# Kernel optimization log

Hardware: AMD Instinct MI355X
Metric: run time of the kernel (lower is better)

The kernel has to match this reference:

```python
import jax, jax.numpy as jnp
import numpy as np

D_MODEL, D_INNER, D_STATE, D_CONV, DT_RANK = 1024, 2048, 16, 4, 64
BATCH, SEQLEN = 4, 2048


def setup_inputs() -> dict:
    key = jax.random.key(0)
    ks = jax.random.split(key, 10)
    def n(k, shape, scale=1.0):
        return (jax.random.normal(k, shape, dtype=jnp.float32) * scale)
    # A_log = log of positive values in (0, d_state] like the torch init
    A_log = jnp.log(jax.random.uniform(ks[7], (D_INNER, D_STATE), dtype=jnp.float32, minval=0.5, maxval=float(D_STATE)))
    return {
        "hidden_states": n(ks[0], (BATCH, SEQLEN, D_MODEL)),
        "in_proj_w": n(ks[1], (2 * D_INNER, D_MODEL), D_MODEL ** -0.5),
        "conv_w": n(ks[2], (D_INNER, D_CONV), D_CONV ** -0.5),
        "conv_b": n(ks[3], (D_INNER,), 0.1),
        "x_proj_w": n(ks[4], (DT_RANK + 2 * D_STATE, D_INNER), D_INNER ** -0.5),
        "dt_proj_w": n(ks[5], (D_INNER, DT_RANK), DT_RANK ** -0.5),
        "dt_proj_b": n(ks[6], (D_INNER,), 0.5),
        "A_log": A_log,
        "D": jnp.ones((D_INNER,), dtype=jnp.float32),
        "out_proj_w": n(ks[8], (D_MODEL, D_INNER), D_INNER ** -0.5),
    }


def _silu(x):
    return x * jax.nn.sigmoid(x)


def _mamba_forward(hidden_states, in_proj_w, conv_w, conv_b, x_proj_w,
                   dt_proj_w, dt_proj_b, A_log, D, out_proj_w):
    B, L, _ = hidden_states.shape
    d_inner, d_conv = conv_w.shape
    d_state = A_log.shape[1]
    dt_rank = dt_proj_w.shape[1]

    # in_proj (no bias): (b, l, 2*d_inner)
    xz = jnp.einsum('bld,ed->ble', hidden_states, in_proj_w)
    x, z = xz[..., :d_inner], xz[..., d_inner:]

    # causal depthwise conv1d (padding = d_conv-1, truncated to L) + SiLU
    x_pad = jnp.pad(x, ((0, 0), (d_conv - 1, 0), (0, 0)))  # (b, L+d_conv-1, d)
    x_conv = sum(x_pad[:, w:w + L, :] * conv_w[:, w] for w in range(d_conv)) + conv_b
    x_conv = _silu(x_conv)  # (b, l, d_inner)

    # x_proj -> dt, B, C
    x_dbl = jnp.einsum('bld,ed->ble', x_conv, x_proj_w)  # (b, l, dt_rank+2*d_state)
    dt_in = x_dbl[..., :dt_rank]
    Bv = x_dbl[..., dt_rank:dt_rank + d_state]  # (b, l, n)
    Cv = x_dbl[..., dt_rank + d_state:]         # (b, l, n)

    delta = jax.nn.softplus(jnp.einsum('blr,dr->bld', dt_in, dt_proj_w) + dt_proj_b)
    A = -jnp.exp(A_log)  # (d, n), entries negative

    # selective scan over time: state h is (b, d, n)
    def step(h, inp):
        d_t, B_t, C_t, u_t = inp  # (b,d), (b,n), (b,n), (b,d)
        dA = jnp.exp(d_t[:, :, None] * A)                          # (b, d, n)
        h = h * dA + (d_t * u_t)[:, :, None] * B_t[:, None, :]     # (b, d, n)
        y = jnp.einsum('bdn,bn->bd', h, C_t)                       # (b, d)
        return h, y

    h0 = jnp.zeros((B, d_inner, d_state), dtype=hidden_states.dtype)
    xs = (jnp.swapaxes(delta, 0, 1), jnp.swapaxes(Bv, 0, 1),
          jnp.swapaxes(Cv, 0, 1), jnp.swapaxes(x_conv, 0, 1))
    _, ys = jax.lax.scan(step, h0, xs)  # (l, b, d)
    y = jnp.swapaxes(ys, 0, 1) + x_conv * D  # skip term D * u
    y = y * _silu(z)                           # gating

    # out_proj (no bias)
    return jnp.einsum('bld,md->blm', y, out_proj_w)


def reference(hidden_states, in_proj_w, conv_w, conv_b, x_proj_w,
              dt_proj_w, dt_proj_b, A_log, D, out_proj_w):
    return _mamba_forward(hidden_states, in_proj_w, conv_w, conv_b, x_proj_w,
                          dt_proj_w, dt_proj_b, A_log, D, out_proj_w)
```

## Files before the change

### kernel.cpp

```cpp
#include <hip/hip_runtime.h>
#include <hip/hip_bf16.h>

constexpr int BATCH = 4, SEQLEN = 2048, DM = 1024, DI = 2048, DS = 16, DC = 4, DTR = 64;
constexpr int M = BATCH * SEQLEN;
constexpr int NXZ = 2 * DI;
constexpr int NXDBL = DTR + 2 * DS;
constexpr int CL = 64;
constexpr int NCH = SEQLEN / CL;
constexpr size_t CS = (size_t)BATCH * DI * DS;
constexpr float L2E = 1.44269504088896f;

typedef __attribute__((ext_vector_type(8))) short short8;
typedef __attribute__((ext_vector_type(4))) float f32x4;

__device__ __forceinline__ float fexp2(float x) { return __builtin_amdgcn_exp2f(x); }
__device__ __forceinline__ float frcp(float x) { return __builtin_amdgcn_rcpf(x); }
__device__ __forceinline__ float fsig(float z) {
  return frcp(1.f + fexp2(-L2E * z));
}
__device__ __forceinline__ float softplus_fast(float x) {
  return (x > 20.f) ? x
                    : 0.693147180559945f * __builtin_amdgcn_logf(1.f + fexp2(x * L2E));
}

__device__ __forceinline__ void load_lds16(const void* g, void* l) {
  __builtin_amdgcn_global_load_lds(
      (const __attribute__((address_space(1))) unsigned int*)g,
      (__attribute__((address_space(3))) unsigned int*)l, 16, 0, 0);
}

__device__ __forceinline__ void vwaitn(int n) {
  switch (n) {
    case 0: asm volatile("s_waitcnt vmcnt(0)" ::: "memory"); break;
    case 2: asm volatile("s_waitcnt vmcnt(2)" ::: "memory"); break;
    case 6: asm volatile("s_waitcnt vmcnt(6)" ::: "memory"); break;
    default: asm volatile("s_waitcnt vmcnt(8)" ::: "memory"); break;
  }
}

__global__ __launch_bounds__(256) void k_cvt(const float* __restrict__ s,
                                             __hip_bfloat16* __restrict__ d, int n) {
  int i = (blockIdx.x * 256 + threadIdx.x) * 4;
  if (i + 3 < n) {
    float4 v = *reinterpret_cast<const float4*>(s + i);
    d[i + 0] = __float2bfloat16(v.x);
    d[i + 1] = __float2bfloat16(v.y);
    d[i + 2] = __float2bfloat16(v.z);
    d[i + 3] = __float2bfloat16(v.w);
  }
}

__global__ __launch_bounds__(256) void k_cvt4(const float* __restrict__ p0, int n0, __hip_bfloat16* __restrict__ q0,
                                              const float* __restrict__ p1, int n1, __hip_bfloat16* __restrict__ q1,
                                              const float* __restrict__ p2, int n2, __hip_bfloat16* __restrict__ q2,
                                              const float* __restrict__ p3, int n3, __hip_bfloat16* __restrict__ q3) {
  int i = (blockIdx.x * 256 + threadIdx.x) * 4;
  const float* s;
  __hip_bfloat16* d;
  if (i < n0) { s = p0; d = q0; }
  else if ((i -= n0) < n1) { s = p1; d = q1; }
  else if ((i -= n1) < n2) { s = p2; d = q2; }
  else if ((i -= n2) < n3) { s = p3; d = q3; }
  else return;
  float4 v = *reinterpret_cast<const float4*>(s + i);
  d[i + 0] = __float2bfloat16(v.x);
  d[i + 1] = __float2bfloat16(v.y);
  d[i + 2] = __float2bfloat16(v.z);
  d[i + 3] = __float2bfloat16(v.w);
}

__global__ __launch_bounds__(256) void k_prepA(const float* __restrict__ alog,
                                               float* __restrict__ an, int n) {
  int i = blockIdx.x * 256 + threadIdx.x;
  if (i < n) an[i] = -__expf(alog[i]) * L2E;
}

__global__ __launch_bounds__(256) void k_prepCW(const float* __restrict__ cw,
                                                float* __restrict__ cwt) {
  int i = blockIdx.x * 256 + threadIdx.x;
  if (i < DI * DC) {
    int d = i >> 2, w = i & 3;
    cwt[w * DI + d] = cw[i];
  }
}

template <int OUTMODE>
__global__ __launch_bounds__(512, 2) void k_gemm8b(const __hip_bfloat16* __restrict__ A, int lda,
                                                   const __hip_bfloat16* __restrict__ Bm, int ldb,
                                                   void* __restrict__ Cp, int ldc, int K) {
  constexpr int BK = 64;
  constexpr int SS = 24576;
  const int tid = threadIdx.x;
  const int wid = tid >> 6, l = tid & 63;
  const int wr = wid >> 2, wc = wid & 3;

  const int gx = gridDim.x;
  int nlin = blockIdx.y * gx + blockIdx.x;
  {
    const int nwg = gx * gridDim.y;
    nlin = (nlin & 7) * (nwg >> 3) + (nlin >> 3);
  }
  const int bm0 = (nlin / gx) * 256, bn0 = (nlin % gx) * 128;
  const int NT = K / BK;

  __shared__ short LDS[3 * SS];

  const int gc8 = (l & 7) ^ ((l >> 3) & 7);
  const __hip_bfloat16* Abase = A + (size_t)(bm0 + wid * 8 + (l >> 3)) * lda + gc8 * 8;
  const __hip_bfloat16* Bbase = Bm + (size_t)(bn0 + wid * 8 + (l >> 3)) * ldb + gc8 * 8;
  const int wslot = wid * 512;

  const int c8k0 = ((l >> 4) ^ (l & 7)) * 8;
  const int c8k1 = ((4 + (l >> 4)) ^ (l & 7)) * 8;
  const int aoff0 = wr * 8192 + (l & 15) * 64;
  const int boff0 = 16384 + (wc * 32 + (l & 15)) * 64;

  f32x4 acc[8][2] = {};
  short8 a[4][2], b[2][2];

  auto stageA = [&](int slot, int kt) {
#pragma unroll
    for (int g = 0; g < 4; g++)
      load_lds16(Abase + (size_t)(g * 64) * lda + kt * BK,
                 &LDS[slot * SS + g * 4096 + wslot]);
  };
  auto stageB = [&](int slot, int kt) {
#pragma unroll
    for (int g = 0; g < 2; g++)
      load_lds16(Bbase + (size_t)(g * 64) * ldb + kt * BK,
                 &LDS[slot * SS + 16384 + g * 4096 + wslot]);
  };

  stageA(0, 0); stageB(0, 0);
  stageA(1, 1); stageB(1, 1);

  for (int t = 0; t < NT; t++) {
    const int slot = t % 3;
    const int sbase = slot * SS;
    const int s2 = (t + 2) % 3;
    const bool pf2 = (t + 2 < NT);
    vwaitn((t + 1 < NT) ? 6 : 0);
    __builtin_amdgcn_s_barrier();
    const int adb = sbase + aoff0;
    const int bdb = sbase + boff0;
#pragma unroll
    for (int i = 0; i < 4; i++) {
      a[i][0] = *reinterpret_cast<const short8*>(&LDS[adb + i * 1024 + c8k0]);
      a[i][1] = *reinterpret_cast<const short8*>(&LDS[adb + i * 1024 + c8k1]);
    }
#pragma unroll
    for (int j = 0; j < 2; j++) {
      b[j][0] = *reinterpret_cast<const short8*>(&LDS[bdb + j * 1024 + c8k0]);
      b[j][1] = *reinterpret_cast<const short8*>(&LDS[bdb + j * 1024 + c8k1]);
    }
    if (pf2) stageA(s2, t + 2);
    __builtin_amdgcn_sched_barrier(0);
    __builtin_amdgcn_s_setprio(1);
#pragma unroll
    for (int i = 0; i < 4; i++)
#pragma unroll
      for (int j = 0; j < 2; j++)
#pragma unroll
        for (int ks = 0; ks < 2; ks++)
          acc[i][j] = __builtin_amdgcn_mfma_f32_16x16x32_bf16(a[i][ks], b[j][ks], acc[i][j], 0, 0, 0);
    __builtin_amdgcn_s_setprio(0);
    __builtin_amdgcn_sched_barrier(0);
#pragma unroll
    for (int i = 0; i < 4; i++) {
      a[i][0] = *reinterpret_cast<const short8*>(&LDS[adb + (4 + i) * 1024 + c8k0]);
      a[i][1] = *reinterpret_cast<const short8*>(&LDS[adb + (4 + i) * 1024 + c8k1]);
    }
    if (pf2) stageB(s2, t + 2);
    __builtin_amdgcn_sched_barrier(0);
    __builtin_amdgcn_s_setprio(1);
#pragma unroll
    for (int i = 0; i < 4; i++)
#pragma unroll
      for (int j = 0; j < 2; j++)
#pragma unroll
        for (int ks = 0; ks < 2; ks++)
          acc[4 + i][j] = __builtin_amdgcn_mfma_f32_16x16x32_bf16(a[i][ks], b[j][ks], acc[4 + i][j], 0, 0, 0);
    __builtin_amdgcn_s_setprio(0);
    __builtin_amdgcn_sched_barrier(0);
  }

  const int crow0 = bm0 + wr * 128 + (l >> 4) * 4;
  const int ccol0 = bn0 + wc * 32 + (l & 15);
#pragma unroll
  for (int im = 0; im < 8; im++)
#pragma unroll
    for (int jn = 0; jn < 2; jn++) {
      const int col = ccol0 + jn * 16;
#pragma unroll
      for (int r = 0; r < 4; r++) {
        const int row = crow0 + im * 16 + r;
        float v = acc[im][jn][r];
        if constexpr (OUTMODE == 0)
          reinterpret_cast<float*>(Cp)[(size_t)row * ldc + col] = v;
        else
          reinterpret_cast<__hip_bfloat16*>(Cp)[(size_t)row * ldc + col] = __float2bfloat16(v);
      }
    }
}

template <int BM, int BN, int OUTMODE>
__global__ __launch_bounds__(256) void k_gemm_dl(const __hip_bfloat16* __restrict__ A, int lda,
                                                 const __hip_bfloat16* __restrict__ Bm, int ldb,
                                                 void* __restrict__ Cp, int ldc, int K,
                                                 const float* __restrict__ bias) {
  constexpr int BK = 32;
  constexpr int WM = BM / 2, WN = BN / 2;
  constexpr int FM = WM / 16, FN = WN / 16;

  const int tid = threadIdx.x;
  const int wid = tid >> 6, lane = tid & 63;
  const int wm = wid >> 1, wn = wid & 1;
  const int bm0 = blockIdx.y * BM, bn0 = blockIdx.x * BN;
  int kz = 0;
  if constexpr (OUTMODE == 4) kz = blockIdx.z;

  __shared__ short As[BM * BK];
  __shared__ short Bs[BN * BK];

  f32x4 acc[FM][FN] = {};

  const int lrow = lane & 15;
  const int lk = (lane >> 4) * 8;
  const int srow = wid * 16 + (lane >> 2);
  const int scol = (lane & 3) * 8;

  const __hip_bfloat16* Ag = &A[(size_t)(bm0 + srow) * lda + scol + (size_t)kz * K];
  const __hip_bfloat16* Bg = &Bm[(size_t)(bn0 + srow) * ldb + scol + (size_t)kz * K];

  for (int k0 = 0; k0 < K; k0 += BK) {
    __syncthreads();
#pragma unroll
    for (int i = 0; i < (BM + 63) / 64; i++)
      load_lds16(Ag + (size_t)i * 64 * lda + k0, &As[(i * 64 + wid * 16) * BK]);
#pragma unroll
    for (int i = 0; i < (BN + 63) / 64; i++)
      if ((BN % 64 == 0) || (i * 64 + wid * 16 < BN))
        load_lds16(Bg + (size_t)i * 64 * ldb + k0, &Bs[(i * 64 + wid * 16) * BK]);
    __syncthreads();

    short8 af[FM], bf[FN];
#pragma unroll
    for (int i = 0; i < FM; i++)
      af[i] = *reinterpret_cast<const short8*>(&As[(wm * WM + i * 16 + lrow) * BK + lk]);
#pragma unroll
    for (int j = 0; j < FN; j++)
      bf[j] = *reinterpret_cast<const short8*>(&Bs[(wn * WN + j * 16 + lrow) * BK + lk]);
#pragma unroll
    for (int i = 0; i < FM; i++)
#pragma unroll
      for (int j = 0; j < FN; j++)
        acc[i][j] = __builtin_amdgcn_mfma_f32_16x16x32_bf16(af[i], bf[j], acc[i][j], 0, 0, 0);
  }

  const int crow0 = bm0 + wm * WM + (lane >> 4) * 4;
  const int ccol0 = bn0 + wn * WN + lrow;
#pragma unroll
  for (int i = 0; i < FM; i++)
#pragma unroll
    for (int j = 0; j < FN; j++) {
      const int col = ccol0 + j * 16;
      float bv = 0.f;
      if constexpr (OUTMODE == 2) bv = bias[col];
#pragma unroll
      for (int r = 0; r < 4; r++) {
        const int row = crow0 + i * 16 + r;
        float v = acc[i][j][r];
        if constexpr (OUTMODE == 0) {
          reinterpret_cast<float*>(Cp)[(size_t)row * ldc + col] = v;
        } else if constexpr (OUTMODE == 2) {
          reinterpret_cast<__hip_bfloat16*>(Cp)[(size_t)row * ldc + col] =
              __float2bfloat16(softplus_fast(v + bv));
        } else {
          reinterpret_cast<float*>(Cp)[(size_t)kz * M * NXDBL + (size_t)row * ldc + col] = v;
        }
      }
    }
}

__global__ __launch_bounds__(256) void k_xred(const float* __restrict__ part,
                                              float* __restrict__ xdbl,
                                              __hip_bfloat16* __restrict__ dtin) {
  int i = (blockIdx.x * 256 + threadIdx.x) * 4;
  float4 s = *reinterpret_cast<const float4*>(part + i);
#pragma unroll
  for (int p = 1; p < 8; p++) {
    const float4 v = *reinterpret_cast<const float4*>(part + (size_t)p * M * NXDBL + i);
    s.x += v.x; s.y += v.y; s.z += v.z; s.w += v.w;
  }
  *reinterpret_cast<float4*>(xdbl + i) = s;
  int c = i % NXDBL;
  if (c < DTR) {
    int m = i / NXDBL;
    __hip_bfloat16* dp = dtin + (size_t)m * DTR + c;
    dp[0] = __float2bfloat16(s.x);
    dp[1] = __float2bfloat16(s.y);
    dp[2] = __float2bfloat16(s.z);
    dp[3] = __float2bfloat16(s.w);
  }
}

__global__ __launch_bounds__(256) void k_conv8(const __hip_bfloat16* __restrict__ xz,
                                               const float* __restrict__ cwt,
                                               const float* __restrict__ cb,
                                               __hip_bfloat16* __restrict__ xc) {
  const int ml = blockIdx.x;
  const int d0 = threadIdx.x * 8;
  const int l = ml & (SEQLEN - 1);
  float acc[8];
  {
    float4 b0 = *reinterpret_cast<const float4*>(cb + d0);
    float4 b1 = *reinterpret_cast<const float4*>(cb + d0 + 4);
    acc[0] = b0.x; acc[1] = b0.y; acc[2] = b0.z; acc[3] = b0.w;
    acc[4] = b1.x; acc[5] = b1.y; acc[6] = b1.z; acc[7] = b1.w;
  }
#pragma unroll
  for (int w = 0; w < DC; w++) {
    int li = l - 3 + w;
    if (li >= 0) {
      short8 xv = *reinterpret_cast<const short8*>(&xz[(size_t)(ml - 3 + w) * NXZ + d0]);
      float4 w0 = *reinterpret_cast<const float4*>(cwt + w * DI + d0);
      float4 w1 = *reinterpret_cast<const float4*>(cwt + w * DI + d0 + 4);
      float wf[8] = {w0.x, w0.y, w0.z, w0.w, w1.x, w1.y, w1.z, w1.w};
#pragma unroll
      for (int j = 0; j < 8; j++) {
        float x = __bfloat162float(__ushort_as_bfloat16((unsigned short)xv[j]));
        acc[j] = fmaf(x, wf[j], acc[j]);
      }
    }
  }
  unsigned short o[8];
#pragma unroll
  for (int j = 0; j < 8; j++)
    o[j] = __bfloat16_as_ushort(__float2bfloat16(acc[j] * fsig(acc[j])));
  *reinterpret_cast<short8*>(&xc[(size_t)ml * DI + d0]) = *reinterpret_cast<short8*>(o);
}

__global__ __launch_bounds__(256) void k_scan1(const __hip_bfloat16* __restrict__ delta_b,
                                               const float* __restrict__ xdbl,
                                               const __hip_bfloat16* __restrict__ xc,
                                               const float* __restrict__ Aneg2,
                                               __hip_bfloat16* __restrict__ Pb,
                                               __hip_bfloat16* __restrict__ Sb) {
  const int tid = threadIdx.x;
  const int d = blockIdx.x * 256 + tid;
  const int c = blockIdx.y, b = blockIdx.z;
  const size_t row0 = (size_t)b * SEQLEN + (size_t)c * CL;

  __shared__ float Bs[CL][16];
  {
    int i = tid * 4;
    int li = i >> 4, n0 = i & 15;
    const float* src = &xdbl[(row0 + li) * NXDBL + DTR + n0];
    *reinterpret_cast<float4*>(&Bs[li][n0]) = *reinterpret_cast<const float4*>(src);
  }

  float Ar[DS];
#pragma unroll
  for (int n = 0; n < DS; n++) Ar[n] = Aneg2[d * DS + n];
  __syncthreads();

  float h[DS] = {};
  float sdelta = 0.f;
  size_t idx = row0 * DI + d;
  float nx_dt = __bfloat162float(delta_b[idx]);
  float nx_u = __bfloat162float(xc[idx]);
  for (int ls = 0; ls < CL; ls++) {
    float delta = nx_dt;
    float u = nx_u;
    if (ls + 1 < CL) {
      size_t idx2 = idx + DI;
      nx_dt = __bfloat162float(delta_b[idx2]);
      nx_u = __bfloat162float(xc[idx2]);
    }
    idx += DI;
    sdelta += delta;
    float du = delta * u;
#pragma unroll
    for (int n = 0; n < DS; n++) {
      float dA = fexp2(delta * Ar[n]);
      h[n] = fmaf(h[n], dA, du * Bs[ls][n]);
    }
  }

  size_t base = (size_t)c * CS + ((size_t)b * DI + d) * DS;
  unsigned short sp[DS], ss[DS];
#pragma unroll
  for (int n = 0; n < DS; n++) {
    ss[n] = __bfloat16_as_ushort(__float2bfloat16(h[n]));
    sp[n] = __bfloat16_as_ushort(__float2bfloat16(fexp2(Ar[n] * sdelta)));
  }
#pragma unroll
  for (int q = 0; q < 2; q++) {
    *reinterpret_cast<short8*>(&Sb[base + q * 8]) = *reinterpret_cast<short8*>(&ss[q * 8]);
    *reinterpret_cast<short8*>(&Pb[base + q * 8]) = *reinterpret_cast<short8*>(&sp[q * 8]);
  }
}

__global__ __launch_bounds__(256) void k_scan2(const __hip_bfloat16* __restrict__ Pb,
                                               const __hip_bfloat16* __restrict__ Sb,
                                               __hip_bfloat16* __restrict__ Hin) {
  size_t t = (size_t)blockIdx.x * 256 + threadIdx.x;
  float h = 0.f;
  for (int c = 0; c < NCH; c++) {
    size_t o = (size_t)c * CS + t;
    Hin[o] = __float2bfloat16(h);
    h = fmaf(__bfloat162float(Pb[o]), h, __bfloat162float(Sb[o]));
  }
}

__global__ __launch_bounds__(256) void k_scan3(const __hip_bfloat16* __restrict__ delta_b,
                                               const float* __restrict__ xdbl,
                                               const __hip_bfloat16* __restrict__ xc,
                                               const __hip_bfloat16* __restrict__ xz,
                                               const float* __restrict__ Aneg2,
                                               const float* __restrict__ Dw,
                                               const __hip_bfloat16* __restrict__ Hin,
                                               __hip_bfloat16* __restrict__ yg) {
  const int tid = threadIdx.x;
  const int d = blockIdx.x * 256 + tid;
  const int c = blockIdx.y, b = blockIdx.z;
  const size_t row0 = (size_t)b * SEQLEN + (size_t)c * CL;

  __shared__ float BCs[CL][32];
  {
    int i = tid * 8;
    int li = i >> 5, n0 = i & 31;
    const float* src = &xdbl[(row0 + li) * NXDBL + DTR + n0];
    *reinterpret_cast<float4*>(&BCs[li][n0]) = *reinterpret_cast<const float4*>(src);
    *reinterpret_cast<float4*>(&BCs[li][n0 + 4]) = *reinterpret_cast<const float4*>(src + 4);
  }

  float Ar[DS];
#pragma unroll
  for (int n = 0; n < DS; n++) Ar[n] = Aneg2[d * DS + n];
  const float Dv = Dw[d];

  float h[DS];
  {
    size_t hbase = (size_t)c * CS + ((size_t)b * DI + d) * DS;
#pragma unroll
    for (int q = 0; q < 2; q++) {
      short8 hv = *reinterpret_cast<const short8*>(&Hin[hbase + q * 8]);
#pragma unroll
      for (int n = 0; n < 8; n++)
        h[q * 8 + n] = __bfloat162float(__ushort_as_bfloat16((unsigned short)hv[n]));
    }
  }
  __syncthreads();

  size_t idx = row0 * DI + d;
  float nx_dt = __bfloat162float(delta_b[idx]);
  float nx_u = __bfloat162float(xc[idx]);
  float nx_z = __bfloat162float(xz[row0 * NXZ + DI + d]);
  for (int ls = 0; ls < CL; ls++) {
    const size_t cur = idx;
    float delta = nx_dt;
    float u = nx_u;
    float zv = nx_z;
    if (ls + 1 < CL) {
      size_t idx2 = idx + DI;
      nx_dt = __bfloat162float(delta_b[idx2]);
      nx_u = __bfloat162float(xc[idx2]);
      nx_z = __bfloat162float(xz[(row0 + ls + 1) * NXZ + DI + d]);
    }
    idx += DI;
    float du = delta * u;
    float y0 = 0.f, y1 = 0.f, y2 = 0.f, y3 = 0.f;
#pragma unroll
    for (int q = 0; q < 4; q++) {
#pragma unroll
      for (int n4 = 0; n4 < 4; n4++) {
        const int n = q * 4 + n4;
        float dA = fexp2(delta * Ar[n]);
        h[n] = fmaf(h[n], dA, du * BCs[ls][n]);
        if (q == 0) y0 = fmaf(h[n], BCs[ls][16 + n], y0);
        else if (q == 1) y1 = fmaf(h[n], BCs[ls][16 + n], y1);
        else if (q == 2) y2 = fmaf(h[n], BCs[ls][16 + n], y2);
        else y3 = fmaf(h[n], BCs[ls][16 + n], y3);
      }
    }
    float y = (y0 + y1) + (y2 + y3);
    float out = (y + u * Dv) * (zv * fsig(zv));
    yg[cur] = __float2bfloat16(out);
  }
}

extern "C" void kernel_launch(void* const* d_in, const int* in_sizes, int n_in,
                              void* d_out, int out_size, void* d_ws, size_t ws_size,
                              hipStream_t stream) {
  const float* hs = (const float*)d_in[0];
  const float* w_in = (const float*)d_in[1];
  const float* conv_w = (const float*)d_in[2];
  const float* conv_b = (const float*)d_in[3];
  const float* w_xp = (const float*)d_in[4];
  const float* w_dt = (const float*)d_in[5];
  const float* dt_b = (const float*)d_in[6];
  const float* A_log = (const float*)d_in[7];
  const float* Dw = (const float*)d_in[8];
  const float* w_out = (const float*)d_in[9];
  float* out = (float*)d_out;

  char* ws = (char*)d_ws;
  size_t off = 0;
  auto alloc = [&](size_t bytes) {
    void* p = ws + off;
    off += (bytes + 255) & ~(size_t)255;
    return p;
  };

  __hip_bfloat16* hs_b   = (__hip_bfloat16*)alloc((size_t)M * DM * 2);
  __hip_bfloat16* win_b  = (__hip_bfloat16*)alloc((size_t)NXZ * DM * 2);
  __hip_bfloat16* wxp_b  = (__hip_bfloat16*)alloc((size_t)NXDBL * DI * 2);
  __hip_bfloat16* wdt_b  = (__hip_bfloat16*)alloc((size_t)DI * DTR * 2);
  __hip_bfloat16* wout_b = (__hip_bfloat16*)alloc((size_t)DM * DI * 2);
  float*          Aneg2  = (float*)alloc((size_t)DI * DS * 4);
  float*          cwt    = (float*)alloc((size_t)DC * DI * 4);
  __hip_bfloat16* xz_b   = (__hip_bfloat16*)alloc((size_t)M * NXZ * 2);
  __hip_bfloat16* xc_b   = (__hip_bfloat16*)alloc((size_t)M * DI * 2);
  float*          xdbl   = (float*)alloc((size_t)M * NXDBL * 4);
  __hip_bfloat16* dtin_b = (__hip_bfloat16*)alloc((size_t)M * DTR * 2);
  __hip_bfloat16* delta_b= (__hip_bfloat16*)alloc((size_t)M * DI * 2);
  __hip_bfloat16* yg_b   = (__hip_bfloat16*)alloc((size_t)M * DI * 2);

  float* xpart = (float*)(ws + 0);
  __hip_bfloat16* Pb  = (__hip_bfloat16*)(ws + 0);
  __hip_bfloat16* Sb  = (__hip_bfloat16*)(ws + ((size_t)8 << 20));
  __hip_bfloat16* Hin = (__hip_bfloat16*)(ws + ((size_t)16 << 20));

  k_cvt<<<(M * DM) / 1024, 256, 0, stream>>>(hs, hs_b, M * DM);
  k_cvt4<<<(NXZ * DM + NXDBL * DI + DI * DTR + DM * DI) / 1024, 256, 0, stream>>>(
      w_in, NXZ * DM, win_b, w_xp, NXDBL * DI, wxp_b, w_dt, DI * DTR, wdt_b,
      w_out, DM * DI, wout_b);
  k_prepA<<<(DI * DS) / 256, 256, 0, stream>>>(A_log, Aneg2, DI * DS);
  k_prepCW<<<(DI * DC + 255) / 256, 256, 0, stream>>>(conv_w, cwt);

  k_gemm8b<1><<<dim3(NXZ / 128, M / 256), 512, 0, stream>>>(
      hs_b, DM, win_b, DM, xz_b, NXZ, DM);

  k_conv8<<<M, 256, 0, stream>>>(xz_b, cwt, conv_b, xc_b);

  k_gemm_dl<64, 96, 4><<<dim3(1, M / 64, 8), 256, 0, stream>>>(
      xc_b, DI, wxp_b, DI, xpart, NXDBL, DI / 8, nullptr);
  k_xred<<<(M * NXDBL) / 1024, 256, 0, stream>>>(xpart, xdbl, dtin_b);

  k_gemm_dl<128, 128, 2><<<dim3(DI / 128, M / 128), 256, 0, stream>>>(
      dtin_b, DTR, wdt_b, DTR, delta_b, DI, DTR, dt_b);

  k_scan1<<<dim3(DI / 256, NCH, BATCH), 256, 0, stream>>>(delta_b, xdbl, xc_b,
                                                          Aneg2, Pb, Sb);
  k_scan2<<<(int)(CS / 256), 256, 0, stream>>>(Pb, Sb, Hin);
  k_scan3<<<dim3(DI / 256, NCH, BATCH), 256, 0, stream>>>(delta_b, xdbl, xc_b,
                                                          xz_b, Aneg2, Dw, Hin, yg_b);

  k_gemm8b<0><<<dim3(DM / 128, M / 256), 512, 0, stream>>>(
      yg_b, DI, wout_b, DI, out, DM, DI);
}
```

Measured before the change: 312.7 us.

## Replace triple-buffered GEMM with double-buffered templated kernel, wider in_proj tile

Rewrites the bf16 MFMA GEMM from a 3-stage, split-stage prefetch pipeline to a simpler 2-stage double buffer that issues the next tile's loads right after the barrier, then loads all fragments before one merged MFMA loop. The kernel is templated on the N tile, and in_proj now uses 256x256 tiles without workgroup swizzling, while out_proj keeps 256x128 with swizzling. The aim is to cut pipeline bookkeeping and, for in_proj, raise data reuse per tile. In exchange it uses a full vmcnt(0) wait each iteration, which may expose more memory latency. It also drops the priority hints and raises register pressure with the wider tile.

```diff
diff --git a/kernel.cpp b/kernel.cpp
--- a/kernel.cpp
+++ b/kernel.cpp
@@ -27,15 +27,6 @@
   __builtin_amdgcn_global_load_lds(
       (const __attribute__((address_space(1))) unsigned int*)g,
       (__attribute__((address_space(3))) unsigned int*)l, 16, 0, 0);
-}
-
-__device__ __forceinline__ void vwaitn(int n) {
-  switch (n) {
-    case 0: asm volatile("s_waitcnt vmcnt(0)" ::: "memory"); break;
-    case 2: asm volatile("s_waitcnt vmcnt(2)" ::: "memory"); break;
-    case 6: asm volatile("s_waitcnt vmcnt(6)" ::: "memory"); break;
-    default: asm volatile("s_waitcnt vmcnt(8)" ::: "memory"); break;
-  }
 }
 
 __global__ __launch_bounds__(256) void k_cvt(const float* __restrict__ s,
@@ -84,26 +75,32 @@
   }
 }
 
-template <int OUTMODE>
-__global__ __launch_bounds__(512, 2) void k_gemm8b(const __hip_bfloat16* __restrict__ A, int lda,
-                                                   const __hip_bfloat16* __restrict__ Bm, int ldb,
-                                                   void* __restrict__ Cp, int ldc, int K) {
+template <int BN, int OUTMODE, bool SWZ>
+__global__ __launch_bounds__(512, 2) void k_gemmp(const __hip_bfloat16* __restrict__ A, int lda,
+                                                  const __hip_bfloat16* __restrict__ Bm, int ldb,
+                                                  void* __restrict__ Cp, int ldc, int K) {
   constexpr int BK = 64;
-  constexpr int SS = 24576;
+  constexpr int ASLOT = 16384;
+  constexpr int BSLOT = BN * BK;
+  constexpr int FN = (BN / 4) / 16;
+  constexpr int BBASE = 2 * ASLOT;
+
   const int tid = threadIdx.x;
   const int wid = tid >> 6, l = tid & 63;
   const int wr = wid >> 2, wc = wid & 3;
 
-  const int gx = gridDim.x;
-  int nlin = blockIdx.y * gx + blockIdx.x;
-  {
+  int bx = blockIdx.x, by = blockIdx.y;
+  if constexpr (SWZ) {
+    const int gx = gridDim.x;
+    int nlin = by * gx + bx;
     const int nwg = gx * gridDim.y;
     nlin = (nlin & 7) * (nwg >> 3) + (nlin >> 3);
-  }
-  const int bm0 = (nlin / gx) * 256, bn0 = (nlin % gx) * 128;
+    by = nlin / gx; bx = nlin % gx;
+  }
+  const int bm0 = by * 256, bn0 = bx * BN;
   const int NT = K / BK;
 
-  __shared__ short LDS[3 * SS];
+  __shared__ short LDS[2 * (ASLOT + BSLOT)];
 
   const int gc8 = (l & 7) ^ ((l >> 3) & 7);
   const __hip_bfloat16* Abase = A + (size_t)(bm0 + wid * 8 + (l >> 3)) * lda + gc8 * 8;
@@ -113,83 +110,66 @@
   const int c8k0 = ((l >> 4) ^ (l & 7)) * 8;
   const int c8k1 = ((4 + (l >> 4)) ^ (l & 7)) * 8;
   const int aoff0 = wr * 8192 + (l & 15) * 64;
-  const int boff0 = 16384 + (wc * 32 + (l & 15)) * 64;
-
-  f32x4 acc[8][2] = {};
-  short8 a[4][2], b[2][2];
-
-  auto stageA = [&](int slot, int kt) {
+  const int boff0 = BBASE + wc * (BN / 4) * 64 + (l & 15) * 64;
+
+  f32x4 acc[8][FN] = {};
+
+  auto stageA = [&](int s, int kt) {
 #pragma unroll
     for (int g = 0; g < 4; g++)
       load_lds16(Abase + (size_t)(g * 64) * lda + kt * BK,
-                 &LDS[slot * SS + g * 4096 + wslot]);
+                 &LDS[s * ASLOT + g * 4096 + wslot]);
   };
-  auto stageB = [&](int slot, int kt) {
-#pragma unroll
-    for (int g = 0; g < 2; g++)
+  auto stageB = [&](int s, int kt) {
+#pragma unroll
+    for (int g = 0; g < BN / 64; g++)
       load_lds16(Bbase + (size_t)(g * 64) * ldb + kt * BK,
-                 &LDS[slot * SS + 16384 + g * 4096 + wslot]);
+                 &LDS[BBASE + s * BSLOT + g * 4096 + wslot]);
   };
 
   stageA(0, 0); stageB(0, 0);
-  stageA(1, 1); stageB(1, 1);
 
   for (int t = 0; t < NT; t++) {
-    const int slot = t % 3;
-    const int sbase = slot * SS;
-    const int s2 = (t + 2) % 3;
-    const bool pf2 = (t + 2 < NT);
-    vwaitn((t + 1 < NT) ? 6 : 0);
+    const int d = t & 1;
+    asm volatile("s_waitcnt vmcnt(0)" ::: "memory");
     __builtin_amdgcn_s_barrier();
-    const int adb = sbase + aoff0;
-    const int bdb = sbase + boff0;
+    if (t + 1 < NT) { stageA(d ^ 1, t + 1); stageB(d ^ 1, t + 1); }
+
+    const int adb = d * ASLOT + aoff0;
+    const int bdb = d * BSLOT + boff0;
+    short8 a0[4][2], a1[4][2], b[FN][2];
 #pragma unroll
     for (int i = 0; i < 4; i++) {
-      a[i][0] = *reinterpret_cast<const short8*>(&LDS[adb + i * 1024 + c8k0]);
-      a[i][1] = *reinterpret_cast<const short8*>(&LDS[adb + i * 1024 + c8k1]);
-    }
-#pragma unroll
-    for (int j = 0; j < 2; j++) {
+      a0[i][0] = *reinterpret_cast<const short8*>(&LDS[adb + i * 1024 + c8k0]);
+      a0[i][1] = *reinterpret_cast<const short8*>(&LDS[adb + i * 1024 + c8k1]);
+    }
+#pragma unroll
+    for (int j = 0; j < FN; j++) {
       b[j][0] = *reinterpret_cast<const short8*>(&LDS[bdb + j * 1024 + c8k0]);
       b[j][1] = *reinterpret_cast<const short8*>(&LDS[bdb + j * 1024 + c8k1]);
     }
-    if (pf2) stageA(s2, t + 2);
-    __builtin_amdgcn_sched_barrier(0);
-    __builtin_amdgcn_s_setprio(1);
+#pragma unroll
+    for (int i = 0; i < 4; i++) {
+      a1[i][0] = *reinterpret_cast<const short8*>(&LDS[adb + (4 + i) * 1024 + c8k0]);
+      a1[i][1] = *reinterpret_cast<const short8*>(&LDS[adb + (4 + i) * 1024 + c8k1]);
+    }
 #pragma unroll
     for (int i = 0; i < 4; i++)
 #pragma unroll
-      for (int j = 0; j < 2; j++)
-#pragma unroll
-        for (int ks = 0; ks < 2; ks++)
-          acc[i][j] = __builtin_amdgcn_mfma_f32_16x16x32_bf16(a[i][ks], b[j][ks], acc[i][j], 0, 0, 0);
-    __builtin_amdgcn_s_setprio(0);
-    __builtin_amdgcn_sched_barrier(0);
-#pragma unroll
-    for (int i = 0; i < 4; i++) {
-      a[i][0] = *reinterpret_cast<const short8*>(&LDS[adb + (4 + i) * 1024 + c8k0]);
-      a[i][1] = *reinterpret_cast<const short8*>(&LDS[adb + (4 + i) * 1024 + c8k1]);
-    }
-    if (pf2) stageB(s2, t + 2);
-    __builtin_amdgcn_sched_barrier(0);
-    __builtin_amdgcn_s_setprio(1);
-#pragma unroll
-    for (int i = 0; i < 4; i++)
-#pragma unroll
-      for (int j = 0; j < 2; j++)
-#pragma unroll
-        for (int ks = 0; ks < 2; ks++)
-          acc[4 + i][j] = __builtin_amdgcn_mfma_f32_16x16x32_bf16(a[i][ks], b[j][ks], acc[4 + i][j], 0, 0, 0);
-    __builtin_amdgcn_s_setprio(0);
-    __builtin_amdgcn_sched_barrier(0);
+      for (int j = 0; j < FN; j++)
+#pragma unroll
+        for (int ks = 0; ks < 2; ks++) {
+          acc[i][j] = __builtin_amdgcn_mfma_f32_16x16x32_bf16(a0[i][ks], b[j][ks], acc[i][j], 0, 0, 0);
+          acc[4 + i][j] = __builtin_amdgcn_mfma_f32_16x16x32_bf16(a1[i][ks], b[j][ks], acc[4 + i][j], 0, 0, 0);
+        }
   }
 
   const int crow0 = bm0 + wr * 128 + (l >> 4) * 4;
-  const int ccol0 = bn0 + wc * 32 + (l & 15);
+  const int ccol0 = bn0 + wc * (BN / 4) + (l & 15);
 #pragma unroll
   for (int im = 0; im < 8; im++)
 #pragma unroll
-    for (int jn = 0; jn < 2; jn++) {
+    for (int jn = 0; jn < FN; jn++) {
       const int col = ccol0 + jn * 16;
 #pragma unroll
       for (int r = 0; r < 4; r++) {
@@ -539,7 +519,7 @@
   k_prepA<<<(DI * DS) / 256, 256, 0, stream>>>(A_log, Aneg2, DI * DS);
   k_prepCW<<<(DI * DC + 255) / 256, 256, 0, stream>>>(conv_w, cwt);
 
-  k_gemm8b<1><<<dim3(NXZ / 128, M / 256), 512, 0, stream>>>(
+  k_gemmp<256, 1, false><<<dim3(NXZ / 256, M / 256), 512, 0, stream>>>(
       hs_b, DM, win_b, DM, xz_b, NXZ, DM);
 
   k_conv8<<<M, 256, 0, stream>>>(xz_b, cwt, conv_b, xc_b);
@@ -557,6 +537,6 @@
   k_scan3<<<dim3(DI / 256, NCH, BATCH), 256, 0, stream>>>(delta_b, xdbl, xc_b,
                                                           xz_b, Aneg2, Dw, Hin, yg_b);
 
-  k_gemm8b<0><<<dim3(DM / 128, M / 256), 512, 0, stream>>>(
+  k_gemmp<128, 0, true><<<dim3(DM / 128, M / 256), 512, 0, stream>>>(
       yg_b, DI, wout_b, DI, out, DM, DI);
 }
```

Measured after the change: 300.0 us. 4.1% less time.
